# Performance work log

Hardware: AMD Instinct MI355X
Metric: run time of the kernel (lower is better)

The kernel has to match this reference:

```python
import jax, jax.numpy as jnp
import numpy as np

N = 524288   # frontier nodes processed this step
D = 8        # max_output_degree (padded children per node)
H = 64       # h_size
X = 128      # x_size


def setup_inputs() -> dict:
    key = jax.random.key(0)
    ks = jax.random.split(key, 8)
    x_embs = jax.random.normal(ks[0], (N, X), dtype=jnp.float32)
    # node-level input mask (1.0 where node has an input word, else 0.0)
    x_mask = (jax.random.uniform(ks[1], (N,)) > 0.3).astype(jnp.float32)
    # hidden states of the already-computed (child) nodes
    h_prev = jax.random.normal(ks[2], (N, H), dtype=jnp.float32)
    # padded child index lists + validity mask (variable out-degree)
    child_idx = jax.random.randint(ks[3], (N, D), 0, N, dtype=jnp.int64)
    child_mask = (jax.random.uniform(ks[4], (N, D)) > 0.5).astype(jnp.float32)
    # parameters
    W_in = jax.random.normal(ks[5], (X, H), dtype=jnp.float32) * 0.05
    b_in = jnp.zeros((H,), dtype=jnp.float32)
    U = jax.random.normal(ks[6], (D, H, H), dtype=jnp.float32) * 0.05  # positional child matrices
    b_aggr = jnp.zeros((H,), dtype=jnp.float32)
    return {
        "x_embs": x_embs, "x_mask": x_mask, "h_prev": h_prev,
        "child_mask": child_mask, "W_in": W_in, "b_in": b_in,
        "U": U, "b_aggr": b_aggr, "child_idx": child_idx,
    }


def reference(x_embs, x_mask, h_prev, child_mask, W_in, b_in, U, b_aggr, child_idx):
    # message + mailbox: gather child hidden states -> [N, D, H], mask padding
    neighbour_h = h_prev[child_idx] * child_mask[..., None]
    # reduce: positional (non-stationary) linear aggregation  h_aggr = sum_p U_p h_p + b
    h_aggr = jnp.einsum("npd,pde->ne", neighbour_h, U) + b_aggr
    # apply: input linear, masked, add aggregate, tanh
    h = (x_embs @ W_in + b_in) * x_mask[:, None] + h_aggr
    return jnp.tanh(h)
```

## Files before the change

### kernel.cpp

```cpp
#include <hip/hip_runtime.h>
#include <hip/hip_bf16.h>

typedef __bf16 bf16x8 __attribute__((ext_vector_type(8)));
typedef float  f32x4  __attribute__((ext_vector_type(4)));
typedef int    i32x4  __attribute__((ext_vector_type(4)));

#define K_N 524288
#define K_D 8
#define K_H 64
#define K_X 128

#define WS_PACKED_SHORTS 40960
#define WS_ZERO_OFF_B    81920
#define WS_NEEDED        82432

__global__ __launch_bounds__(64) void treernn_prepack(
    const float* __restrict__ W_in,
    const float* __restrict__ U,
    short* __restrict__ wsPacked,
    float* __restrict__ zerop)
{
    const int f = blockIdx.x;
    const int lane = threadIdx.x;
    if (f == 80) {
        zerop[lane] = 0.0f;
        zerop[lane + 64] = 0.0f;
        return;
    }
    const int g = lane >> 4;
    const int c = lane & 15;
    bf16x8 v;
    if (f < 16) {
        const int ks = f >> 2, ct = f & 3;
        #pragma unroll
        for (int j = 0; j < 8; ++j) {
            const int k = ks * 32 + 8 * g + j;
            v[j] = (__bf16)W_in[k * K_H + ct * 16 + c];
        }
    } else {
        const int f2 = f - 16;
        const int p = f2 >> 3, ks = (f2 >> 2) & 1, ct = f2 & 3;
        #pragma unroll
        for (int j = 0; j < 8; ++j) {
            const int k = ks * 32 + 8 * g + j;
            v[j] = (__bf16)U[p * K_H * K_H + k * K_H + ct * 16 + c];
        }
    }
    *reinterpret_cast<bf16x8*>(wsPacked + ((size_t)f * 64 + lane) * 8) = v;
}

__global__ __launch_bounds__(512, 4) void treernn_main(
    const float* __restrict__ x_embs,
    const float* __restrict__ x_mask,
    const float* __restrict__ h_prev,
    const float* __restrict__ child_mask,
    const float* __restrict__ b_in,
    const float* __restrict__ b_aggr,
    const int*   __restrict__ child_idx,
    const short* __restrict__ wsPacked,
    const float* __restrict__ zerop,
    float* __restrict__ out)
{
    __shared__ __align__(16) short lds[WS_PACKED_SHORTS];

    {
        const i32x4* src = reinterpret_cast<const i32x4*>(wsPacked);
        i32x4* dst = reinterpret_cast<i32x4*>(lds);
        #pragma unroll
        for (int i = 0; i < 10; ++i)
            dst[threadIdx.x + i * 512] = src[threadIdx.x + i * 512];
    }

    const int lane = threadIdx.x & 63;
    const int wave = threadIdx.x >> 6;
    const int g = lane >> 4;
    const int c = lane & 15;
    const int base = (blockIdx.x * 8 + wave) * 32;

    int   idxs[2][8];
    float cms[2][8];
    #pragma unroll
    for (int rt = 0; rt < 2; ++rt) {
        const int node = base + rt * 16 + c;
        const i32x4* ip = reinterpret_cast<const i32x4*>(child_idx + (size_t)node * K_D);
        const i32x4 i0 = ip[0], i1 = ip[1];
        idxs[rt][0] = i0[0]; idxs[rt][1] = i0[1]; idxs[rt][2] = i0[2]; idxs[rt][3] = i0[3];
        idxs[rt][4] = i1[0]; idxs[rt][5] = i1[1]; idxs[rt][6] = i1[2]; idxs[rt][7] = i1[3];
        const f32x4* mp = reinterpret_cast<const f32x4*>(child_mask + (size_t)node * K_D);
        const f32x4 m0 = mp[0], m1 = mp[1];
        cms[rt][0] = m0[0]; cms[rt][1] = m0[1]; cms[rt][2] = m0[2]; cms[rt][3] = m0[3];
        cms[rt][4] = m1[0]; cms[rt][5] = m1[1]; cms[rt][6] = m1[2]; cms[rt][7] = m1[3];
    }

    f32x4 xmv[2];
    float xmrow[2];
    #pragma unroll
    for (int rt = 0; rt < 2; ++rt) {
        xmv[rt] = *reinterpret_cast<const f32x4*>(x_mask + base + rt * 16 + 4 * g);
        xmrow[rt] = x_mask[base + rt * 16 + c];
    }

    f32x4 buf[2][2][4];

    #pragma unroll
    for (int rt = 0; rt < 2; ++rt) {
        const float* src = (cms[rt][0] != 0.0f) ? (h_prev + (size_t)idxs[rt][0] * K_H) : zerop;
        buf[0][rt][0] = *reinterpret_cast<const f32x4*>(src + 8 * g);
        buf[0][rt][1] = *reinterpret_cast<const f32x4*>(src + 8 * g + 4);
        buf[0][rt][2] = *reinterpret_cast<const f32x4*>(src + 32 + 8 * g);
        buf[0][rt][3] = *reinterpret_cast<const f32x4*>(src + 32 + 8 * g + 4);
    }

    f32x4 acc[2][4];
    #pragma unroll
    for (int rt = 0; rt < 2; ++rt)
        #pragma unroll
        for (int ct = 0; ct < 4; ++ct) {
            f32x4 z = {0.0f, 0.0f, 0.0f, 0.0f};
            acc[rt][ct] = z;
        }

    __syncthreads();

    #pragma unroll
    for (int rt = 0; rt < 2; ++rt) {
        const float* src = (cms[rt][1] != 0.0f) ? (h_prev + (size_t)idxs[rt][1] * K_H) : zerop;
        buf[1][rt][0] = *reinterpret_cast<const f32x4*>(src + 8 * g);
        buf[1][rt][1] = *reinterpret_cast<const f32x4*>(src + 8 * g + 4);
        buf[1][rt][2] = *reinterpret_cast<const f32x4*>(src + 32 + 8 * g);
        buf[1][rt][3] = *reinterpret_cast<const f32x4*>(src + 32 + 8 * g + 4);
    }

    {
        #pragma unroll
        for (int rt = 0; rt < 2; ++rt) {
            const float* src = (xmrow[rt] != 0.0f) ? (x_embs + (size_t)(base + rt * 16 + c) * K_X) : zerop;
            #pragma unroll
            for (int ks = 0; ks < 4; ++ks) {
                const f32x4 a0 = *reinterpret_cast<const f32x4*>(src + ks * 32 + 8 * g);
                const f32x4 a1 = *reinterpret_cast<const f32x4*>(src + ks * 32 + 8 * g + 4);
                bf16x8 af;
                #pragma unroll
                for (int j = 0; j < 4; ++j) {
                    af[j]     = (__bf16)a0[j];
                    af[j + 4] = (__bf16)a1[j];
                }
                #pragma unroll
                for (int ct = 0; ct < 4; ++ct) {
                    const bf16x8 wf = *reinterpret_cast<const bf16x8*>(&lds[((ks * 4 + ct) * 64 + lane) * 8]);
                    acc[rt][ct] = __builtin_amdgcn_mfma_f32_16x16x32_bf16(af, wf, acc[rt][ct], 0, 0, 0);
                }
            }
        }
    }

    #pragma unroll
    for (int p = 0; p < 8; ++p) {
        const int pb = p & 1;

        bf16x8 a0[2], a1[2];
        #pragma unroll
        for (int rt = 0; rt < 2; ++rt) {
            #pragma unroll
            for (int j = 0; j < 4; ++j) {
                a0[rt][j]     = (__bf16)buf[pb][rt][0][j];
                a0[rt][j + 4] = (__bf16)buf[pb][rt][1][j];
                a1[rt][j]     = (__bf16)buf[pb][rt][2][j];
                a1[rt][j + 4] = (__bf16)buf[pb][rt][3][j];
            }
        }

        if (p < 6) {
            const int q = p + 2;
            #pragma unroll
            for (int rt = 0; rt < 2; ++rt) {
                const float* src = (cms[rt][q] != 0.0f) ? (h_prev + (size_t)idxs[rt][q] * K_H) : zerop;
                buf[pb][rt][0] = *reinterpret_cast<const f32x4*>(src + 8 * g);
                buf[pb][rt][1] = *reinterpret_cast<const f32x4*>(src + 8 * g + 4);
                buf[pb][rt][2] = *reinterpret_cast<const f32x4*>(src + 32 + 8 * g);
                buf[pb][rt][3] = *reinterpret_cast<const f32x4*>(src + 32 + 8 * g + 4);
            }
        }

        bf16x8 uf[2][4];
        #pragma unroll
        for (int ks = 0; ks < 2; ++ks)
            #pragma unroll
            for (int ct = 0; ct < 4; ++ct)
                uf[ks][ct] = *reinterpret_cast<const bf16x8*>(&lds[8192 + ((p * 8 + ks * 4 + ct) * 64 + lane) * 8]);

        #pragma unroll
        for (int rt = 0; rt < 2; ++rt) {
            #pragma unroll
            for (int ct = 0; ct < 4; ++ct)
                acc[rt][ct] = __builtin_amdgcn_mfma_f32_16x16x32_bf16(a0[rt], uf[0][ct], acc[rt][ct], 0, 0, 0);
            #pragma unroll
            for (int ct = 0; ct < 4; ++ct)
                acc[rt][ct] = __builtin_amdgcn_mfma_f32_16x16x32_bf16(a1[rt], uf[1][ct], acc[rt][ct], 0, 0, 0);
        }
    }

    #pragma unroll
    for (int ct = 0; ct < 4; ++ct) {
        const int col = ct * 16 + c;
        const float bi = b_in[col];
        const float ba = b_aggr[col];
        #pragma unroll
        for (int rt = 0; rt < 2; ++rt) {
            #pragma unroll
            for (int j = 0; j < 4; ++j) {
                const int node = base + rt * 16 + 4 * g + j;
                const float xm = xmv[rt][j];
                float h = acc[rt][ct][j] + ba + ((xm != 0.0f) ? bi : 0.0f);
                h = fminf(fmaxf(h, -9.0f), 9.0f);
                const float ex = __expf(2.0f * h);
                out[(size_t)node * K_H + col] = (ex - 1.0f) / (ex + 1.0f);
            }
        }
    }
}

__global__ void treernn_naive(
    const float* __restrict__ x_embs, const float* __restrict__ x_mask,
    const float* __restrict__ h_prev, const float* __restrict__ child_mask,
    const float* __restrict__ W_in,   const float* __restrict__ b_in,
    const float* __restrict__ U,      const float* __restrict__ b_aggr,
    const int*   __restrict__ child_idx, float* __restrict__ out)
{
    const int n = blockIdx.x * 4 + (threadIdx.x >> 6);
    const int e = threadIdx.x & 63;
    if (n >= K_N) return;
    float s = 0.0f;
    const float xm = x_mask[n];
    if (xm != 0.0f) {
        for (int k = 0; k < K_X; ++k) s += x_embs[(size_t)n * K_X + k] * W_in[k * K_H + e];
        s += b_in[e];
    }
    float a = b_aggr[e];
    for (int p = 0; p < K_D; ++p) {
        const float cm = child_mask[n * K_D + p];
        if (cm != 0.0f) {
            const int id = child_idx[n * K_D + p];
            const float* hp = h_prev + (size_t)id * K_H;
            for (int d = 0; d < K_H; ++d) a += hp[d] * U[p * K_H * K_H + d * K_H + e];
        }
    }
    float h = s + a;
    h = fminf(fmaxf(h, -9.0f), 9.0f);
    const float ex = __expf(2.0f * h);
    out[(size_t)n * K_H + e] = (ex - 1.0f) / (ex + 1.0f);
}

extern "C" void kernel_launch(void* const* d_in, const int* in_sizes, int n_in,
                              void* d_out, int out_size, void* d_ws, size_t ws_size,
                              hipStream_t stream) {
    const float* x_embs     = (const float*)d_in[0];
    const float* x_mask     = (const float*)d_in[1];
    const float* h_prev     = (const float*)d_in[2];
    const float* child_mask = (const float*)d_in[3];
    const float* W_in       = (const float*)d_in[4];
    const float* b_in       = (const float*)d_in[5];
    const float* U          = (const float*)d_in[6];
    const float* b_aggr     = (const float*)d_in[7];
    const int*   child_idx  = (const int*)d_in[8];
    float* out = (float*)d_out;

    if (d_ws != nullptr && ws_size >= (size_t)WS_NEEDED) {
        short* wsPacked = (short*)d_ws;
        float* zerop    = (float*)((char*)d_ws + WS_ZERO_OFF_B);
        treernn_prepack<<<81, 64, 0, stream>>>(W_in, U, wsPacked, zerop);
        treernn_main<<<K_N / 256, 512, 0, stream>>>(x_embs, x_mask, h_prev, child_mask,
                                                    b_in, b_aggr, child_idx,
                                                    wsPacked, zerop, out);
    } else {
        treernn_naive<<<K_N / 4, 256, 0, stream>>>(x_embs, x_mask, h_prev, child_mask,
                                                   W_in, b_in, U, b_aggr, child_idx, out);
    }
}
```

Baseline: 191.7 us.

## Pre-convert h_prev to bf16 in workspace to halve gather traffic

Adds a pass that converts the whole h_prev table to bf16 in a large workspace buffer. The main kernel then gathers 128-byte bf16 rows instead of 256-byte fp32 rows and skips the per-child conversion. It also switches x_embs loads and output stores to nontemporal hints. The extra conversion pass reads 128 MB and writes 64 MB each call, and the new path runs only if the harness supplies a workspace of about 64 MB.

```diff
diff --git a/kernel.cpp b/kernel.cpp
--- a/kernel.cpp
+++ b/kernel.cpp
@@ -12,7 +12,9 @@
 
 #define WS_PACKED_SHORTS 40960
 #define WS_ZERO_OFF_B    81920
-#define WS_NEEDED        82432
+#define WS_HB_OFF_B      131072
+#define WS_NEEDED_MED    82432
+#define WS_NEEDED_BIG    (131072 + (size_t)K_N * K_H * 2)
 
 __global__ __launch_bounds__(64) void treernn_prepack(
     const float* __restrict__ W_in,
@@ -49,7 +51,186 @@
     *reinterpret_cast<bf16x8*>(wsPacked + ((size_t)f * 64 + lane) * 8) = v;
 }
 
-__global__ __launch_bounds__(512, 4) void treernn_main(
+__global__ __launch_bounds__(512) void treernn_h2bf16(
+    const float* __restrict__ h_prev,
+    __bf16* __restrict__ hb)
+{
+    const size_t tid = (size_t)blockIdx.x * 512 + threadIdx.x;
+    const f32x4* s = reinterpret_cast<const f32x4*>(h_prev) + 2 * tid;
+    const f32x4 v0 = s[0], v1 = s[1];
+    bf16x8 o;
+    #pragma unroll
+    for (int j = 0; j < 4; ++j) {
+        o[j]     = (__bf16)v0[j];
+        o[j + 4] = (__bf16)v1[j];
+    }
+    reinterpret_cast<bf16x8*>(hb)[tid] = o;
+}
+
+__global__ __launch_bounds__(512, 4) void treernn_main_bf16(
+    const float* __restrict__ x_embs,
+    const float* __restrict__ x_mask,
+    const __bf16* __restrict__ hb,
+    const float* __restrict__ child_mask,
+    const float* __restrict__ b_in,
+    const float* __restrict__ b_aggr,
+    const int*   __restrict__ child_idx,
+    const short* __restrict__ wsPacked,
+    const float* __restrict__ zerop,
+    float* __restrict__ out)
+{
+    __shared__ __align__(16) short lds[WS_PACKED_SHORTS];
+
+    {
+        const i32x4* src = reinterpret_cast<const i32x4*>(wsPacked);
+        i32x4* dst = reinterpret_cast<i32x4*>(lds);
+        #pragma unroll
+        for (int i = 0; i < 10; ++i)
+            dst[threadIdx.x + i * 512] = src[threadIdx.x + i * 512];
+    }
+
+    const int lane = threadIdx.x & 63;
+    const int wave = threadIdx.x >> 6;
+    const int g = lane >> 4;
+    const int c = lane & 15;
+    const int base = (blockIdx.x * 8 + wave) * 32;
+    const bf16x8* zb = reinterpret_cast<const bf16x8*>(zerop);
+
+    int   idxs[2][8];
+    float cms[2][8];
+    #pragma unroll
+    for (int rt = 0; rt < 2; ++rt) {
+        const int node = base + rt * 16 + c;
+        const i32x4* ip = reinterpret_cast<const i32x4*>(child_idx + (size_t)node * K_D);
+        const i32x4 i0 = ip[0], i1 = ip[1];
+        idxs[rt][0] = i0[0]; idxs[rt][1] = i0[1]; idxs[rt][2] = i0[2]; idxs[rt][3] = i0[3];
+        idxs[rt][4] = i1[0]; idxs[rt][5] = i1[1]; idxs[rt][6] = i1[2]; idxs[rt][7] = i1[3];
+        const f32x4* mp = reinterpret_cast<const f32x4*>(child_mask + (size_t)node * K_D);
+        const f32x4 m0 = mp[0], m1 = mp[1];
+        cms[rt][0] = m0[0]; cms[rt][1] = m0[1]; cms[rt][2] = m0[2]; cms[rt][3] = m0[3];
+        cms[rt][4] = m1[0]; cms[rt][5] = m1[1]; cms[rt][6] = m1[2]; cms[rt][7] = m1[3];
+    }
+
+    f32x4 xmv[2];
+    float xmrow[2];
+    #pragma unroll
+    for (int rt = 0; rt < 2; ++rt) {
+        xmv[rt] = *reinterpret_cast<const f32x4*>(x_mask + base + rt * 16 + 4 * g);
+        xmrow[rt] = x_mask[base + rt * 16 + c];
+    }
+
+    bf16x8 buf[2][2][2];
+
+    #pragma unroll
+    for (int rt = 0; rt < 2; ++rt) {
+        const bf16x8* src = (cms[rt][0] != 0.0f)
+            ? reinterpret_cast<const bf16x8*>(hb + (size_t)idxs[rt][0] * K_H) : zb;
+        buf[0][rt][0] = src[g];
+        buf[0][rt][1] = src[4 + g];
+    }
+
+    f32x4 acc[2][4];
+    #pragma unroll
+    for (int rt = 0; rt < 2; ++rt)
+        #pragma unroll
+        for (int ct = 0; ct < 4; ++ct) {
+            f32x4 z = {0.0f, 0.0f, 0.0f, 0.0f};
+            acc[rt][ct] = z;
+        }
+
+    __syncthreads();
+
+    #pragma unroll
+    for (int rt = 0; rt < 2; ++rt) {
+        const bf16x8* src = (cms[rt][1] != 0.0f)
+            ? reinterpret_cast<const bf16x8*>(hb + (size_t)idxs[rt][1] * K_H) : zb;
+        buf[1][rt][0] = src[g];
+        buf[1][rt][1] = src[4 + g];
+    }
+
+    {
+        #pragma unroll
+        for (int rt = 0; rt < 2; ++rt) {
+            const float* src = (xmrow[rt] != 0.0f) ? (x_embs + (size_t)(base + rt * 16 + c) * K_X) : zerop;
+            #pragma unroll
+            for (int ks = 0; ks < 4; ++ks) {
+                const f32x4 a0 = __builtin_nontemporal_load(reinterpret_cast<const f32x4*>(src + ks * 32 + 8 * g));
+                const f32x4 a1 = __builtin_nontemporal_load(reinterpret_cast<const f32x4*>(src + ks * 32 + 8 * g + 4));
+                bf16x8 af;
+                #pragma unroll
+                for (int j = 0; j < 4; ++j) {
+                    af[j]     = (__bf16)a0[j];
+                    af[j + 4] = (__bf16)a1[j];
+                }
+                #pragma unroll
+                for (int ct = 0; ct < 4; ++ct) {
+                    const bf16x8 wf = *reinterpret_cast<const bf16x8*>(&lds[((ks * 4 + ct) * 64 + lane) * 8]);
+                    acc[rt][ct] = __builtin_amdgcn_mfma_f32_16x16x32_bf16(af, wf, acc[rt][ct], 0, 0, 0);
+                }
+            }
+        }
+    }
+
+    #pragma unroll
+    for (int p = 0; p < 8; ++p) {
+        const int pb = p & 1;
+
+        const bf16x8 a0_0 = buf[pb][0][0], a1_0 = buf[pb][0][1];
+        const bf16x8 a0_1 = buf[pb][1][0], a1_1 = buf[pb][1][1];
+
+        if (p < 6) {
+            const int q = p + 2;
+            #pragma unroll
+            for (int rt = 0; rt < 2; ++rt) {
+                const bf16x8* src = (cms[rt][q] != 0.0f)
+                    ? reinterpret_cast<const bf16x8*>(hb + (size_t)idxs[rt][q] * K_H) : zb;
+                buf[pb][rt][0] = src[g];
+                buf[pb][rt][1] = src[4 + g];
+            }
+        }
+
+        bf16x8 uf[2][4];
+        #pragma unroll
+        for (int ks = 0; ks < 2; ++ks)
+            #pragma unroll
+            for (int ct = 0; ct < 4; ++ct)
+                uf[ks][ct] = *reinterpret_cast<const bf16x8*>(&lds[8192 + ((p * 8 + ks * 4 + ct) * 64 + lane) * 8]);
+
+        #pragma unroll
+        for (int ct = 0; ct < 4; ++ct)
+            acc[0][ct] = __builtin_amdgcn_mfma_f32_16x16x32_bf16(a0_0, uf[0][ct], acc[0][ct], 0, 0, 0);
+        #pragma unroll
+        for (int ct = 0; ct < 4; ++ct)
+            acc[0][ct] = __builtin_amdgcn_mfma_f32_16x16x32_bf16(a1_0, uf[1][ct], acc[0][ct], 0, 0, 0);
+        #pragma unroll
+        for (int ct = 0; ct < 4; ++ct)
+            acc[1][ct] = __builtin_amdgcn_mfma_f32_16x16x32_bf16(a0_1, uf[0][ct], acc[1][ct], 0, 0, 0);
+        #pragma unroll
+        for (int ct = 0; ct < 4; ++ct)
+            acc[1][ct] = __builtin_amdgcn_mfma_f32_16x16x32_bf16(a1_1, uf[1][ct], acc[1][ct], 0, 0, 0);
+    }
+
+    #pragma unroll
+    for (int ct = 0; ct < 4; ++ct) {
+        const int col = ct * 16 + c;
+        const float bi = b_in[col];
+        const float ba = b_aggr[col];
+        #pragma unroll
+        for (int rt = 0; rt < 2; ++rt) {
+            #pragma unroll
+            for (int j = 0; j < 4; ++j) {
+                const int node = base + rt * 16 + 4 * g + j;
+                const float xm = xmv[rt][j];
+                float h = acc[rt][ct][j] + ba + ((xm != 0.0f) ? bi : 0.0f);
+                h = fminf(fmaxf(h, -9.0f), 9.0f);
+                const float ex = __expf(2.0f * h);
+                __builtin_nontemporal_store((ex - 1.0f) / (ex + 1.0f), &out[(size_t)node * K_H + col]);
+            }
+        }
+    }
+}
+
+__global__ __launch_bounds__(512, 4) void treernn_main_f32(
     const float* __restrict__ x_embs,
     const float* __restrict__ x_mask,
     const float* __restrict__ h_prev,
@@ -62,7 +243,6 @@
     float* __restrict__ out)
 {
     __shared__ __align__(16) short lds[WS_PACKED_SHORTS];
-
     {
         const i32x4* src = reinterpret_cast<const i32x4*>(wsPacked);
         i32x4* dst = reinterpret_cast<i32x4*>(lds);
@@ -70,7 +250,6 @@
         for (int i = 0; i < 10; ++i)
             dst[threadIdx.x + i * 512] = src[threadIdx.x + i * 512];
     }
-
     const int lane = threadIdx.x & 63;
     const int wave = threadIdx.x >> 6;
     const int g = lane >> 4;
@@ -91,7 +270,6 @@
         cms[rt][0] = m0[0]; cms[rt][1] = m0[1]; cms[rt][2] = m0[2]; cms[rt][3] = m0[3];
         cms[rt][4] = m1[0]; cms[rt][5] = m1[1]; cms[rt][6] = m1[2]; cms[rt][7] = m1[3];
     }
-
     f32x4 xmv[2];
     float xmrow[2];
     #pragma unroll
@@ -99,9 +277,7 @@
         xmv[rt] = *reinterpret_cast<const f32x4*>(x_mask + base + rt * 16 + 4 * g);
         xmrow[rt] = x_mask[base + rt * 16 + c];
     }
-
     f32x4 buf[2][2][4];
-
     #pragma unroll
     for (int rt = 0; rt < 2; ++rt) {
         const float* src = (cms[rt][0] != 0.0f) ? (h_prev + (size_t)idxs[rt][0] * K_H) : zerop;
@@ -110,7 +286,6 @@
         buf[0][rt][2] = *reinterpret_cast<const f32x4*>(src + 32 + 8 * g);
         buf[0][rt][3] = *reinterpret_cast<const f32x4*>(src + 32 + 8 * g + 4);
     }
-
     f32x4 acc[2][4];
     #pragma unroll
     for (int rt = 0; rt < 2; ++rt)
@@ -119,9 +294,7 @@
             f32x4 z = {0.0f, 0.0f, 0.0f, 0.0f};
             acc[rt][ct] = z;
         }
-
     __syncthreads();
-
     #pragma unroll
     for (int rt = 0; rt < 2; ++rt) {
         const float* src = (cms[rt][1] != 0.0f) ? (h_prev + (size_t)idxs[rt][1] * K_H) : zerop;
@@ -130,7 +303,6 @@
         buf[1][rt][2] = *reinterpret_cast<const f32x4*>(src + 32 + 8 * g);
         buf[1][rt][3] = *reinterpret_cast<const f32x4*>(src + 32 + 8 * g + 4);
     }
-
     {
         #pragma unroll
         for (int rt = 0; rt < 2; ++rt) {
@@ -153,11 +325,9 @@
             }
         }
     }
-
     #pragma unroll
     for (int p = 0; p < 8; ++p) {
         const int pb = p & 1;
-
         bf16x8 a0[2], a1[2];
         #pragma unroll
         for (int rt = 0; rt < 2; ++rt) {
@@ -169,7 +339,6 @@
                 a1[rt][j + 4] = (__bf16)buf[pb][rt][3][j];
             }
         }
-
         if (p < 6) {
             const int q = p + 2;
             #pragma unroll
@@ -181,14 +350,12 @@
                 buf[pb][rt][3] = *reinterpret_cast<const f32x4*>(src + 32 + 8 * g + 4);
             }
         }
-
         bf16x8 uf[2][4];
         #pragma unroll
         for (int ks = 0; ks < 2; ++ks)
             #pragma unroll
             for (int ct = 0; ct < 4; ++ct)
                 uf[ks][ct] = *reinterpret_cast<const bf16x8*>(&lds[8192 + ((p * 8 + ks * 4 + ct) * 64 + lane) * 8]);
-
         #pragma unroll
         for (int rt = 0; rt < 2; ++rt) {
             #pragma unroll
@@ -199,7 +366,6 @@
                 acc[rt][ct] = __builtin_amdgcn_mfma_f32_16x16x32_bf16(a1[rt], uf[1][ct], acc[rt][ct], 0, 0, 0);
         }
     }
-
     #pragma unroll
     for (int ct = 0; ct < 4; ++ct) {
         const int col = ct * 16 + c;
@@ -265,13 +431,22 @@
     const int*   child_idx  = (const int*)d_in[8];
     float* out = (float*)d_out;
 
-    if (d_ws != nullptr && ws_size >= (size_t)WS_NEEDED) {
+    if (d_ws != nullptr && ws_size >= WS_NEEDED_BIG) {
+        short*  wsPacked = (short*)d_ws;
+        float*  zerop    = (float*)((char*)d_ws + WS_ZERO_OFF_B);
+        __bf16* hb       = (__bf16*)((char*)d_ws + WS_HB_OFF_B);
+        treernn_prepack<<<81, 64, 0, stream>>>(W_in, U, wsPacked, zerop);
+        treernn_h2bf16<<<K_N * K_H / 8 / 512, 512, 0, stream>>>(h_prev, hb);
+        treernn_main_bf16<<<K_N / 256, 512, 0, stream>>>(x_embs, x_mask, hb, child_mask,
+                                                         b_in, b_aggr, child_idx,
+                                                         wsPacked, zerop, out);
+    } else if (d_ws != nullptr && ws_size >= (size_t)WS_NEEDED_MED) {
         short* wsPacked = (short*)d_ws;
         float* zerop    = (float*)((char*)d_ws + WS_ZERO_OFF_B);
         treernn_prepack<<<81, 64, 0, stream>>>(W_in, U, wsPacked, zerop);
-        treernn_main<<<K_N / 256, 512, 0, stream>>>(x_embs, x_mask, h_prev, child_mask,
-                                                    b_in, b_aggr, child_idx,
-                                                    wsPacked, zerop, out);
+        treernn_main_f32<<<K_N / 256, 512, 0, stream>>>(x_embs, x_mask, h_prev, child_mask,
+                                                        b_in, b_aggr, child_idx,
+                                                        wsPacked, zerop, out);
     } else {
         treernn_naive<<<K_N / 4, 256, 0, stream>>>(x_embs, x_mask, h_prev, child_mask,
                                                    W_in, b_in, U, b_aggr, child_idx, out);
```

After: 155.1 us. 1.24x faster.
